# Kernel optimization log

Measured on AMD Instinct MI355X. Metric: run time of the kernel, lower is better.

## Reference

```python
import jax, jax.numpy as jnp
import numpy as np
from jax import lax

DN = ('NCHW', 'OIHW', 'NCHW')


def setup_inputs() -> dict:
    key = jax.random.key(0)
    k1, k2, k3, k4, k5, k6 = jax.random.split(key, 6)
    B, Ch, H, W = 16, 256, 32, 32   # two feature maps of 256 ch -> c = 512
    C = 2 * Ch
    return {
        'x1': jax.random.normal(k1, (B, Ch, H, W), dtype=jnp.float32),
        'x2': jax.random.normal(k2, (B, Ch, H, W), dtype=jnp.float32),
        'g_w': jax.random.normal(k3, (C, C, 3, 3), dtype=jnp.float32) * 0.02,
        'w_w': jax.random.normal(k4, (256, C, 1, 1), dtype=jnp.float32) * 0.05,
        'weight1': jax.random.normal(k5, (C, 16), dtype=jnp.float32) * 0.1,
        'weight2': jax.random.normal(k6, (C, 16), dtype=jnp.float32) * 0.1,
    }


def reference(x1, x2, g_w, w_w, weight1, weight2):
    x = jnp.concatenate([x1, x2], axis=1)            # [b, c, h, w]
    b, c, h, w = x.shape
    g_x = lax.conv_general_dilated(x, g_w, (1, 1), 'SAME', dimension_numbers=DN)
    value = g_x.reshape(b, c, h * w)                 # [b, c, n]
    q = x.reshape(b, c, h * w)                       # query == key source
    sim = jnp.einsum('bcn,bdn->bcd', q, q) * (float(c) ** -0.5)  # [b, c, c]
    random_map = weight1 @ weight2.T                 # [c, c]
    attn = jax.nn.softmax(sim + random_map[None], axis=-1)
    ctx = jnp.einsum('bcd,bdn->bcn', attn, value).reshape(b, c, h, w)
    out = lax.conv_general_dilated(ctx, w_w, (1, 1), 'VALID', dimension_numbers=DN)
    return out
```

## Files before the change

kernel.cpp:

```cpp
#include <hip/hip_runtime.h>
#include <math.h>

typedef float f32x4 __attribute__((ext_vector_type(4)));
typedef short s16x8 __attribute__((ext_vector_type(8)));
typedef unsigned int u32;
typedef unsigned short u16;
typedef u16 u16x4 __attribute__((ext_vector_type(4)));

static constexpr size_t OFF_XT    = 0;
static constexpr size_t OFF_XQ    = 4734976;
static constexpr size_t OFF_ATTNT = 4734976;
static constexpr size_t OFF_WATTN = 6832128;
static constexpr size_t OFF_P0    = 8929280;
static constexpr size_t OFF_P1    = 11026432;
static constexpr size_t OFF_VT    = 8929280;
static constexpr size_t OFF_WA    = 13123584;
static constexpr size_t OFF_RM    = 14303232;
static constexpr size_t OFF_WWB   = 14565376;

__device__ __forceinline__ u16 f2bf(float f) {
    u32 u = __float_as_uint(f);
    u32 r = (u + 0x7FFFu + ((u >> 16) & 1u)) >> 16;
    return (u16)r;
}
__device__ __forceinline__ float bf2f(u16 v) {
    return __uint_as_float(((u32)v) << 16);
}

__device__ __forceinline__ void gload_lds16(const void* g, void* l) {
    __builtin_amdgcn_global_load_lds(
        (const u32 __attribute__((address_space(1)))*)(uintptr_t)g,
        (u32 __attribute__((address_space(3)))*)(uintptr_t)l, 16, 0, 0);
}

__global__ __launch_bounds__(256) void prep_kernel(const float* __restrict__ x1,
                                                   const float* __restrict__ x2,
                                                   const float* __restrict__ gw,
                                                   const float* __restrict__ ww,
                                                   const float* __restrict__ w1,
                                                   const float* __restrict__ w2,
                                                   float* __restrict__ rm,
                                                   u16* __restrict__ wA,
                                                   u16* __restrict__ wwb,
                                                   u16* __restrict__ xT,
                                                   u16* __restrict__ xq) {
    __shared__ __attribute__((aligned(16))) u32 shm[4608];
    const int t = threadIdx.x;
    const int bid = blockIdx.x;

    if (bid < 512) {
        const int co = bid;
        const float* g = gw + (size_t)co * 4608;
        float* lf = (float*)shm;
#pragma unroll
        for (int i = 0; i < 18; ++i) lf[t + i * 256] = g[t + i * 256];
        __syncthreads();
        u16* dst = wA + (size_t)co * 4608;
#pragma unroll
        for (int i = 0; i < 18; ++i) {
            int k = t + i * 256;
            int r = k >> 9, ci = k & 511;
            dst[k] = f2bf(lf[ci * 9 + r]);
        }
    } else if (bid < 2560) {
        int xid = bid - 512;
        int nt = xid & 15;
        int cit = (xid >> 4) & 7;
        int b = xid >> 7;
        int n0 = nt * 64, ci0 = cit * 64;
        const float* src = (ci0 < 256) ? (x1 + ((size_t)(b * 256 + ci0)) * 1024)
                                       : (x2 + ((size_t)(b * 256 + ci0 - 256)) * 1024);
        u16* xqb = xq + ((size_t)(b * 512 + ci0)) * 1024;
        u16* lt = (u16*)shm;
#pragma unroll
        for (int p4 = 0; p4 < 4; ++p4) {
            int ch = (t >> 4) + p4 * 16;
            int px = (t & 15) * 4;
            float4 v = *(const float4*)&src[(size_t)ch * 1024 + n0 + px];
            u16x4 pk = {f2bf(v.x), f2bf(v.y), f2bf(v.z), f2bf(v.w)};
            *(u16x4*)&xqb[(size_t)ch * 1024 + n0 + px] = pk;
            lt[(px + 0) * 65 + ch] = pk[0];
            lt[(px + 1) * 65 + ch] = pk[1];
            lt[(px + 2) * 65 + ch] = pk[2];
            lt[(px + 3) * 65 + ch] = pk[3];
        }
        __syncthreads();
        {
            int px_l = t >> 2, c16 = (t & 3) * 16;
            int n = n0 + px_l;
            int y = n >> 5, x = n & 31;
            int p = (y + 1) * 34 + (x + 1);
            u16* dst = xT + ((size_t)b * 1156 + p) * 512 + ci0 + c16;
            *(s16x8*)&dst[0] = *(const s16x8*)&lt[px_l * 65 + c16];
            *(s16x8*)&dst[8] = *(const s16x8*)&lt[px_l * 65 + c16 + 8];
        }
    } else if (bid < 2576) {
        int b = bid - 2560;
        u16* base = xT + (size_t)b * 1156 * 512;
        s16x8 z = {0, 0, 0, 0, 0, 0, 0, 0};
        for (int idx = t; idx < 132 * 64; idx += 256) {
            int row = idx >> 6, seg = idx & 63;
            int p;
            if (row < 34) p = row;
            else if (row < 68) p = 1122 + (row - 34);
            else if (row < 100) p = (row - 67) * 34;
            else p = (row - 99) * 34 + 33;
            *(s16x8*)&base[(size_t)p * 512 + seg * 8] = z;
        }
    } else if (bid < 3600) {
        int idx = (bid - 2576) * 256 + t;
        int c = idx >> 9, d = idx & 511;
        float s = 0.f;
#pragma unroll
        for (int k = 0; k < 16; ++k) s = fmaf(w1[c * 16 + k], w2[d * 16 + k], s);
        rm[idx] = s;
    } else {
        int idx = (bid - 3600) * 256 + t;
        float4 v = ((const float4*)ww)[idx];
        u16x4 pk = {f2bf(v.x), f2bf(v.y), f2bf(v.z), f2bf(v.w)};
        *(u16x4*)&wwb[(size_t)idx * 4] = pk;
    }
}

__global__ __launch_bounds__(256) void sim_part(const u16* __restrict__ xq,
                                                u16* __restrict__ simP) {
    __shared__ __attribute__((aligned(16))) u16 smem[128 * 128];
    u16* As = smem;
    u16* Bs = smem + 128 * 64;
    const int b = blockIdx.z, m0 = blockIdx.y * 128;
    const int n0 = (blockIdx.x & 3) * 128, khalf = blockIdx.x >> 2;
    const int t = threadIdx.x, w = t >> 6, l = t & 63;
    const u16* xb = xq + (size_t)b * 512 * 1024 + khalf * 512;

    const u16 *agp[4], *bgp[4];
    u16 *ald[4], *bld[4];
#pragma unroll
    for (int i = 0; i < 4; ++i) {
        int rr = w * 8 + i * 32 + (l >> 3);
        int gi = (l & 7) ^ (rr & 7);
        agp[i] = xb + (size_t)(m0 + rr) * 1024 + gi * 8;
        bgp[i] = xb + (size_t)(n0 + rr) * 1024 + gi * 8;
        ald[i] = &As[(w * 8 + i * 32) * 64];
        bld[i] = &Bs[(w * 8 + i * 32) * 64];
    }

    f32x4 acc[4][4] = {};
    const int wm = (w >> 1) * 64, wn = (w & 1) * 64;

    for (int kt = 0; kt < 8; ++kt) {
        int ko = kt << 6;
        if (kt) __syncthreads();
#pragma unroll
        for (int i = 0; i < 4; ++i) gload_lds16(agp[i] + ko, ald[i]);
#pragma unroll
        for (int i = 0; i < 4; ++i) gload_lds16(bgp[i] + ko, bld[i]);
        __syncthreads();
#pragma unroll
        for (int kk = 0; kk < 2; ++kk) {
            int gbase = kk * 4 + (l >> 4);
            s16x8 af[4], bf[4];
#pragma unroll
            for (int i = 0; i < 4; ++i) {
                int row = wm + i * 16 + (l & 15);
                af[i] = *(const s16x8*)&As[row * 64 + ((gbase ^ (row & 7)) << 3)];
            }
#pragma unroll
            for (int j = 0; j < 4; ++j) {
                int row = wn + j * 16 + (l & 15);
                bf[j] = *(const s16x8*)&Bs[row * 64 + ((gbase ^ (row & 7)) << 3)];
            }
#pragma unroll
            for (int i = 0; i < 4; ++i)
#pragma unroll
                for (int j = 0; j < 4; ++j)
                    acc[i][j] = __builtin_amdgcn_mfma_f32_16x16x32_bf16(af[i], bf[j], acc[i][j], 0, 0, 0);
        }
    }

    __syncthreads();
    const int col = l & 15, r4 = (l >> 4) * 4;
#pragma unroll
    for (int i = 0; i < 4; ++i)
#pragma unroll
        for (int j = 0; j < 4; ++j) {
            int n_l = wn + j * 16 + col;
            int m_b = wm + i * 16 + r4;
            u16x4 pk = {f2bf(acc[i][j][0]), f2bf(acc[i][j][1]),
                        f2bf(acc[i][j][2]), f2bf(acc[i][j][3])};
            *(u16x4*)&smem[n_l * 128 + (m_b ^ ((n_l & 15) << 3))] = pk;
        }
    __syncthreads();
    u16* sTb = simP + (size_t)khalf * 4194304 + (size_t)b * 512 * 512;
    {
        int n_l = t >> 1;
#pragma unroll
        for (int rep = 0; rep < 8; ++rep) {
            int c0 = (((t & 1) + rep * 2) << 3);
            s16x8 v = *(const s16x8*)&smem[n_l * 128 + (c0 ^ ((n_l & 15) << 3))];
            *(s16x8*)&sTb[(size_t)(n0 + n_l) * 512 + m0 + c0] = v;
        }
    }
}

__global__ __launch_bounds__(256) void finish_kernel(const u16* __restrict__ p0,
                                                     const u16* __restrict__ p1,
                                                     const float* __restrict__ rm,
                                                     u16* __restrict__ attnT) {
    __shared__ float rml[32 * 513];
    __shared__ float scr[256];
    const int t = threadIdx.x;
    const int b = blockIdx.x >> 4, c0 = (blockIdx.x & 15) * 32;
    const int cl = t & 31, g = t >> 5;
    const float scale = 0.04419417382415922f;

    for (int idx = t; idx < 32 * 512; idx += 256) {
        int c_l = idx >> 9, d = idx & 511;
        rml[c_l * 513 + d] = rm[(size_t)(c0 + c_l) * 512 + d];
    }
    __syncthreads();

    const u16* q0 = p0 + (size_t)b * 262144 + c0 + cl;
    const u16* q1 = p1 + (size_t)b * 262144 + c0 + cl;
    u16* ap = attnT + (size_t)b * 262144 + c0 + cl;
    const float* rp = &rml[cl * 513];

    float e[64];
    float s = 0.f;
#pragma unroll
    for (int dd = 0; dd < 64; ++dd) {
        int d = g * 64 + dd;
        float v = (bf2f(q0[(size_t)d * 512]) + bf2f(q1[(size_t)d * 512])) * scale + rp[d];
        e[dd] = __expf(v);
        s += e[dd];
    }
    scr[t] = s;
    __syncthreads();
    float tot = 0.f;
#pragma unroll
    for (int k = 0; k < 8; ++k) tot += scr[k * 32 + cl];
    float inv = 1.f / tot;
#pragma unroll
    for (int dd = 0; dd < 64; ++dd) {
        int d = g * 64 + dd;
        ap[(size_t)d * 512] = f2bf(e[dd] * inv);
    }
}

__global__ __launch_bounds__(256) void conv_gemm(const u16* __restrict__ wA,
                                                 const u16* __restrict__ xT,
                                                 u16* __restrict__ vT) {
    __shared__ __attribute__((aligned(16))) u16 smem[128 * 128];
    u16* As = smem;
    u16* Bs = smem + 128 * 64;
    const int b = blockIdx.z, m0 = blockIdx.y * 128, n0 = blockIdx.x * 128;
    const int t = threadIdx.x, w = t >> 6, l = t & 63;
    const u16* xTb = xT + (size_t)b * 1156 * 512;

    int gi[4], pb[4];
    const u16* agp[4];
    u16 *ald[4], *bld[4];
#pragma unroll
    for (int i = 0; i < 4; ++i) {
        int rr = w * 8 + i * 32 + (l >> 3);
        gi[i] = (l & 7) ^ (rr & 7);
        agp[i] = wA + (size_t)(m0 + rr) * 4608 + gi[i] * 8;
        int n = n0 + rr;
        pb[i] = (n >> 5) * 34 + (n & 31);
        ald[i] = &As[(w * 8 + i * 32) * 64];
        bld[i] = &Bs[(w * 8 + i * 32) * 64];
    }

    f32x4 acc[4][4] = {};
    const int wm = (w >> 1) * 64, wn = (w & 1) * 64;

    for (int kt = 0; kt < 72; ++kt) {
        int r = kt >> 3, ci0k = (kt & 7) << 6;
        int rdiv3 = (r * 11) >> 5;
        int poff = rdiv3 * 34 + (r - rdiv3 * 3);
        int aofs = r * 512 + ci0k;
        if (kt) __syncthreads();
#pragma unroll
        for (int i = 0; i < 4; ++i) gload_lds16(agp[i] + aofs, ald[i]);
#pragma unroll
        for (int i = 0; i < 4; ++i)
            gload_lds16(xTb + (size_t)(pb[i] + poff) * 512 + ci0k + gi[i] * 8, bld[i]);
        __syncthreads();

#pragma unroll
        for (int kk = 0; kk < 2; ++kk) {
            int gbase = kk * 4 + (l >> 4);
            s16x8 af[4], bf[4];
#pragma unroll
            for (int i = 0; i < 4; ++i) {
                int row = wm + i * 16 + (l & 15);
                af[i] = *(const s16x8*)&As[row * 64 + ((gbase ^ (row & 7)) << 3)];
            }
#pragma unroll
            for (int j = 0; j < 4; ++j) {
                int row = wn + j * 16 + (l & 15);
                bf[j] = *(const s16x8*)&Bs[row * 64 + ((gbase ^ (row & 7)) << 3)];
            }
#pragma unroll
            for (int i = 0; i < 4; ++i)
#pragma unroll
                for (int j = 0; j < 4; ++j)
                    acc[i][j] = __builtin_amdgcn_mfma_f32_16x16x32_bf16(af[i], bf[j], acc[i][j], 0, 0, 0);
        }
    }

    __syncthreads();
    const int col = l & 15, r4 = (l >> 4) * 4;
#pragma unroll
    for (int i = 0; i < 4; ++i)
#pragma unroll
        for (int j = 0; j < 4; ++j) {
            int n_l = wn + j * 16 + col;
            int co_b = wm + i * 16 + r4;
            u16x4 pk = {f2bf(acc[i][j][0]), f2bf(acc[i][j][1]),
                        f2bf(acc[i][j][2]), f2bf(acc[i][j][3])};
            *(u16x4*)&smem[n_l * 128 + (co_b ^ ((n_l & 15) << 3))] = pk;
        }
    __syncthreads();
    u16* vTb = vT + (size_t)b * 1024 * 512;
    {
        int n_l = t >> 1;
#pragma unroll
        for (int rep = 0; rep < 8; ++rep) {
            int c0 = (((t & 1) + rep * 2) << 3);
            s16x8 v = *(const s16x8*)&smem[n_l * 128 + (c0 ^ ((n_l & 15) << 3))];
            *(s16x8*)&vTb[(size_t)(n0 + n_l) * 512 + m0 + c0] = v;
        }
    }
}

template <int MODE>
__global__ __launch_bounds__(256) void gemm_nt(const u16* __restrict__ A, size_t sA,
                                               const u16* __restrict__ B, size_t sB,
                                               void* __restrict__ Cv, size_t sC,
                                               int K, int ldc) {
    __shared__ __attribute__((aligned(16))) u16 As[128 * 64];
    __shared__ __attribute__((aligned(16))) u16 Bs[128 * 64];
    const int b = blockIdx.z, m0 = blockIdx.y * 128, n0 = blockIdx.x * 128;
    const int t = threadIdx.x, w = t >> 6, l = t & 63;
    const u16* Ab = A + (size_t)b * sA;
    const u16* Bb = B + (size_t)b * sB;

    const u16 *agp[4], *bgp[4];
    u16 *ald[4], *bld[4];
#pragma unroll
    for (int i = 0; i < 4; ++i) {
        int rr = w * 8 + i * 32 + (l >> 3);
        int gi = (l & 7) ^ (rr & 7);
        agp[i] = Ab + (size_t)(m0 + rr) * K + gi * 8;
        bgp[i] = Bb + (size_t)(n0 + rr) * K + gi * 8;
        ald[i] = &As[(w * 8 + i * 32) * 64];
        bld[i] = &Bs[(w * 8 + i * 32) * 64];
    }

    f32x4 acc[4][4] = {};
    const int wm = (w >> 1) * 64, wn = (w & 1) * 64;
    const int nkt = K >> 6;
    for (int kt = 0; kt < nkt; ++kt) {
        int ko = kt << 6;
        if (kt) __syncthreads();
#pragma unroll
        for (int i = 0; i < 4; ++i) gload_lds16(agp[i] + ko, ald[i]);
#pragma unroll
        for (int i = 0; i < 4; ++i) gload_lds16(bgp[i] + ko, bld[i]);
        __syncthreads();
#pragma unroll
        for (int kk = 0; kk < 2; ++kk) {
            int gbase = kk * 4 + (l >> 4);
            s16x8 af[4], bf[4];
#pragma unroll
            for (int i = 0; i < 4; ++i) {
                int row = wm + i * 16 + (l & 15);
                af[i] = *(const s16x8*)&As[row * 64 + ((gbase ^ (row & 7)) << 3)];
            }
#pragma unroll
            for (int j = 0; j < 4; ++j) {
                int row = wn + j * 16 + (l & 15);
                bf[j] = *(const s16x8*)&Bs[row * 64 + ((gbase ^ (row & 7)) << 3)];
            }
#pragma unroll
            for (int i = 0; i < 4; ++i)
#pragma unroll
                for (int j = 0; j < 4; ++j)
                    acc[i][j] = __builtin_amdgcn_mfma_f32_16x16x32_bf16(af[i], bf[j], acc[i][j], 0, 0, 0);
        }
    }

    const int col = l & 15, r4 = (l >> 4) * 4;
#pragma unroll
    for (int i = 0; i < 4; ++i)
#pragma unroll
        for (int j = 0; j < 4; ++j)
#pragma unroll
            for (int reg = 0; reg < 4; ++reg) {
                int m = m0 + wm + i * 16 + r4 + reg;
                int n = n0 + wn + j * 16 + col;
                if (MODE == 1) {
                    u16* C = (u16*)Cv + (size_t)b * sC;
                    C[(size_t)m * ldc + n] = f2bf(acc[i][j][reg]);
                } else {
                    float* C = (float*)Cv + (size_t)b * sC;
                    C[(size_t)m * ldc + n] = acc[i][j][reg];
                }
            }
}

extern "C" void kernel_launch(void* const* d_in, const int* in_sizes, int n_in,
                              void* d_out, int out_size, void* d_ws, size_t ws_size,
                              hipStream_t stream) {
    (void)in_sizes; (void)n_in; (void)out_size; (void)ws_size;
    const float* x1 = (const float*)d_in[0];
    const float* x2 = (const float*)d_in[1];
    const float* gw = (const float*)d_in[2];
    const float* ww = (const float*)d_in[3];
    const float* w1 = (const float*)d_in[4];
    const float* w2 = (const float*)d_in[5];
    float* out = (float*)d_out;
    float* ws = (float*)d_ws;

    u16* xT    = (u16*)(ws + OFF_XT);
    u16* xq    = (u16*)(ws + OFF_XQ);
    u16* attnT = (u16*)(ws + OFF_ATTNT);
    u16* wattn = (u16*)(ws + OFF_WATTN);
    u16* simP  = (u16*)(ws + OFF_P0);
    u16* p0    = (u16*)(ws + OFF_P0);
    u16* p1    = (u16*)(ws + OFF_P1);
    u16* vT    = (u16*)(ws + OFF_VT);
    u16* wA    = (u16*)(ws + OFF_WA);
    float* rm  = ws + OFF_RM;
    u16* wwb   = (u16*)(ws + OFF_WWB);

    prep_kernel<<<3728, 256, 0, stream>>>(x1, x2, gw, ww, w1, w2, rm, wA, wwb, xT, xq);
    sim_part<<<dim3(8, 4, 16), 256, 0, stream>>>(xq, simP);
    finish_kernel<<<256, 256, 0, stream>>>(p0, p1, rm, attnT);
    gemm_nt<1><<<dim3(4, 2, 16), 256, 0, stream>>>(
        wwb, 0, attnT, (size_t)512 * 512, wattn, (size_t)256 * 512, 512, 512);
    conv_gemm<<<dim3(8, 4, 16), 256, 0, stream>>>(wA, xT, vT);
    gemm_nt<2><<<dim3(8, 2, 16), 256, 0, stream>>>(
        wattn, (size_t)256 * 512, vT, (size_t)1024 * 512, out, (size_t)256 * 1024, 512, 1024);
}
```

Measured before the change: 222.3 us.

## Fuse sim and conv GEMMs into one concurrent launch with separate vT buffer

Merges the similarity partial GEMM and the 3x3 conv implicit GEMM into a single launch, splitting the grid by blockIdx.x so both sets of blocks run concurrently. vT moves to its own workspace region so it no longer aliases the sim partial buffers that finish_kernel reads. The aim is to fill the GPU better, overlap the two independent GEMMs and drop one launch. The fused path needs a larger workspace and falls back to the old sequence when the workspace is too small.

Result: slower. 275.2 us (+23.8%).

```diff
diff --git a/kernel.cpp b/kernel.cpp
--- a/kernel.cpp
+++ b/kernel.cpp
@@ -17,6 +17,7 @@
 static constexpr size_t OFF_WA    = 13123584;
 static constexpr size_t OFF_RM    = 14303232;
 static constexpr size_t OFF_WWB   = 14565376;
+static constexpr size_t OFF_VT2   = 14630912;
 
 __device__ __forceinline__ u16 f2bf(float f) {
     u32 u = __float_as_uint(f);
@@ -122,13 +123,14 @@
     }
 }
 
-__global__ __launch_bounds__(256) void sim_part(const u16* __restrict__ xq,
-                                                u16* __restrict__ simP) {
-    __shared__ __attribute__((aligned(16))) u16 smem[128 * 128];
+__device__ __forceinline__ void sim_body(u16* __restrict__ smem,
+                                         const u16* __restrict__ xq,
+                                         u16* __restrict__ simP,
+                                         int bx, int by, int bz) {
     u16* As = smem;
     u16* Bs = smem + 128 * 64;
-    const int b = blockIdx.z, m0 = blockIdx.y * 128;
-    const int n0 = (blockIdx.x & 3) * 128, khalf = blockIdx.x >> 2;
+    const int b = bz, m0 = by * 128;
+    const int n0 = (bx & 3) * 128, khalf = bx >> 2;
     const int t = threadIdx.x, w = t >> 6, l = t & 63;
     const u16* xb = xq + (size_t)b * 512 * 1024 + khalf * 512;
 
@@ -200,6 +202,118 @@
             *(s16x8*)&sTb[(size_t)(n0 + n_l) * 512 + m0 + c0] = v;
         }
     }
+}
+
+__device__ __forceinline__ void conv_body(u16* __restrict__ smem,
+                                          const u16* __restrict__ wA,
+                                          const u16* __restrict__ xT,
+                                          u16* __restrict__ vT,
+                                          int bx, int by, int bz) {
+    u16* As = smem;
+    u16* Bs = smem + 128 * 64;
+    const int b = bz, m0 = by * 128, n0 = bx * 128;
+    const int t = threadIdx.x, w = t >> 6, l = t & 63;
+    const u16* xTb = xT + (size_t)b * 1156 * 512;
+
+    int gi[4], pb[4];
+    const u16* agp[4];
+    u16 *ald[4], *bld[4];
+#pragma unroll
+    for (int i = 0; i < 4; ++i) {
+        int rr = w * 8 + i * 32 + (l >> 3);
+        gi[i] = (l & 7) ^ (rr & 7);
+        agp[i] = wA + (size_t)(m0 + rr) * 4608 + gi[i] * 8;
+        int n = n0 + rr;
+        pb[i] = (n >> 5) * 34 + (n & 31);
+        ald[i] = &As[(w * 8 + i * 32) * 64];
+        bld[i] = &Bs[(w * 8 + i * 32) * 64];
+    }
+
+    f32x4 acc[4][4] = {};
+    const int wm = (w >> 1) * 64, wn = (w & 1) * 64;
+
+    for (int kt = 0; kt < 72; ++kt) {
+        int r = kt >> 3, ci0k = (kt & 7) << 6;
+        int rdiv3 = (r * 11) >> 5;
+        int poff = rdiv3 * 34 + (r - rdiv3 * 3);
+        int aofs = r * 512 + ci0k;
+        if (kt) __syncthreads();
+#pragma unroll
+        for (int i = 0; i < 4; ++i) gload_lds16(agp[i] + aofs, ald[i]);
+#pragma unroll
+        for (int i = 0; i < 4; ++i)
+            gload_lds16(xTb + (size_t)(pb[i] + poff) * 512 + ci0k + gi[i] * 8, bld[i]);
+        __syncthreads();
+
+#pragma unroll
+        for (int kk = 0; kk < 2; ++kk) {
+            int gbase = kk * 4 + (l >> 4);
+            s16x8 af[4], bf[4];
+#pragma unroll
+            for (int i = 0; i < 4; ++i) {
+                int row = wm + i * 16 + (l & 15);
+                af[i] = *(const s16x8*)&As[row * 64 + ((gbase ^ (row & 7)) << 3)];
+            }
+#pragma unroll
+            for (int j = 0; j < 4; ++j) {
+                int row = wn + j * 16 + (l & 15);
+                bf[j] = *(const s16x8*)&Bs[row * 64 + ((gbase ^ (row & 7)) << 3)];
+            }
+#pragma unroll
+            for (int i = 0; i < 4; ++i)
+#pragma unroll
+                for (int j = 0; j < 4; ++j)
+                    acc[i][j] = __builtin_amdgcn_mfma_f32_16x16x32_bf16(af[i], bf[j], acc[i][j], 0, 0, 0);
+        }
+    }
+
+    __syncthreads();
+    const int col = l & 15, r4 = (l >> 4) * 4;
+#pragma unroll
+    for (int i = 0; i < 4; ++i)
+#pragma unroll
+        for (int j = 0; j < 4; ++j) {
+            int n_l = wn + j * 16 + col;
+            int co_b = wm + i * 16 + r4;
+            u16x4 pk = {f2bf(acc[i][j][0]), f2bf(acc[i][j][1]),
+                        f2bf(acc[i][j][2]), f2bf(acc[i][j][3])};
+            *(u16x4*)&smem[n_l * 128 + (co_b ^ ((n_l & 15) << 3))] = pk;
+        }
+    __syncthreads();
+    u16* vTb = vT + (size_t)b * 1024 * 512;
+    {
+        int n_l = t >> 1;
+#pragma unroll
+        for (int rep = 0; rep < 8; ++rep) {
+            int c0 = (((t & 1) + rep * 2) << 3);
+            s16x8 v = *(const s16x8*)&smem[n_l * 128 + (c0 ^ ((n_l & 15) << 3))];
+            *(s16x8*)&vTb[(size_t)(n0 + n_l) * 512 + m0 + c0] = v;
+        }
+    }
+}
+
+__global__ __launch_bounds__(256) void sim_part(const u16* __restrict__ xq,
+                                                u16* __restrict__ simP) {
+    __shared__ __attribute__((aligned(16))) u16 smem[128 * 128];
+    sim_body(smem, xq, simP, blockIdx.x, blockIdx.y, blockIdx.z);
+}
+__global__ __launch_bounds__(256) void conv_gemm(const u16* __restrict__ wA,
+                                                 const u16* __restrict__ xT,
+                                                 u16* __restrict__ vT) {
+    __shared__ __attribute__((aligned(16))) u16 smem[128 * 128];
+    conv_body(smem, wA, xT, vT, blockIdx.x, blockIdx.y, blockIdx.z);
+}
+
+__global__ __launch_bounds__(256) void sim_conv_fused(const u16* __restrict__ xq,
+                                                      u16* __restrict__ simP,
+                                                      const u16* __restrict__ wA,
+                                                      const u16* __restrict__ xT,
+                                                      u16* __restrict__ vT) {
+    __shared__ __attribute__((aligned(16))) u16 smem[128 * 128];
+    if (blockIdx.x < 8)
+        conv_body(smem, wA, xT, vT, blockIdx.x, blockIdx.y, blockIdx.z);
+    else
+        sim_body(smem, xq, simP, blockIdx.x - 8, blockIdx.y, blockIdx.z);
 }
 
 __global__ __launch_bounds__(256) void finish_kernel(const u16* __restrict__ p0,
@@ -243,93 +357,6 @@
     for (int dd = 0; dd < 64; ++dd) {
         int d = g * 64 + dd;
         ap[(size_t)d * 512] = f2bf(e[dd] * inv);
-    }
-}
-
-__global__ __launch_bounds__(256) void conv_gemm(const u16* __restrict__ wA,
-                                                 const u16* __restrict__ xT,
-                                                 u16* __restrict__ vT) {
-    __shared__ __attribute__((aligned(16))) u16 smem[128 * 128];
-    u16* As = smem;
-    u16* Bs = smem + 128 * 64;
-    const int b = blockIdx.z, m0 = blockIdx.y * 128, n0 = blockIdx.x * 128;
-    const int t = threadIdx.x, w = t >> 6, l = t & 63;
-    const u16* xTb = xT + (size_t)b * 1156 * 512;
-
-    int gi[4], pb[4];
-    const u16* agp[4];
-    u16 *ald[4], *bld[4];
-#pragma unroll
-    for (int i = 0; i < 4; ++i) {
-        int rr = w * 8 + i * 32 + (l >> 3);
-        gi[i] = (l & 7) ^ (rr & 7);
-        agp[i] = wA + (size_t)(m0 + rr) * 4608 + gi[i] * 8;
-        int n = n0 + rr;
-        pb[i] = (n >> 5) * 34 + (n & 31);
-        ald[i] = &As[(w * 8 + i * 32) * 64];
-        bld[i] = &Bs[(w * 8 + i * 32) * 64];
-    }
-
-    f32x4 acc[4][4] = {};
-    const int wm = (w >> 1) * 64, wn = (w & 1) * 64;
-
-    for (int kt = 0; kt < 72; ++kt) {
-        int r = kt >> 3, ci0k = (kt & 7) << 6;
-        int rdiv3 = (r * 11) >> 5;
-        int poff = rdiv3 * 34 + (r - rdiv3 * 3);
-        int aofs = r * 512 + ci0k;
-        if (kt) __syncthreads();
-#pragma unroll
-        for (int i = 0; i < 4; ++i) gload_lds16(agp[i] + aofs, ald[i]);
-#pragma unroll
-        for (int i = 0; i < 4; ++i)
-            gload_lds16(xTb + (size_t)(pb[i] + poff) * 512 + ci0k + gi[i] * 8, bld[i]);
-        __syncthreads();
-
-#pragma unroll
-        for (int kk = 0; kk < 2; ++kk) {
-            int gbase = kk * 4 + (l >> 4);
-            s16x8 af[4], bf[4];
-#pragma unroll
-            for (int i = 0; i < 4; ++i) {
-                int row = wm + i * 16 + (l & 15);
-                af[i] = *(const s16x8*)&As[row * 64 + ((gbase ^ (row & 7)) << 3)];
-            }
-#pragma unroll
-            for (int j = 0; j < 4; ++j) {
-                int row = wn + j * 16 + (l & 15);
-                bf[j] = *(const s16x8*)&Bs[row * 64 + ((gbase ^ (row & 7)) << 3)];
-            }
-#pragma unroll
-            for (int i = 0; i < 4; ++i)
-#pragma unroll
-                for (int j = 0; j < 4; ++j)
-                    acc[i][j] = __builtin_amdgcn_mfma_f32_16x16x32_bf16(af[i], bf[j], acc[i][j], 0, 0, 0);
-        }
-    }
-
-    __syncthreads();
-    const int col = l & 15, r4 = (l >> 4) * 4;
-#pragma unroll
-    for (int i = 0; i < 4; ++i)
-#pragma unroll
-        for (int j = 0; j < 4; ++j) {
-            int n_l = wn + j * 16 + col;
-            int co_b = wm + i * 16 + r4;
-            u16x4 pk = {f2bf(acc[i][j][0]), f2bf(acc[i][j][1]),
-                        f2bf(acc[i][j][2]), f2bf(acc[i][j][3])};
-            *(u16x4*)&smem[n_l * 128 + (co_b ^ ((n_l & 15) << 3))] = pk;
-        }
-    __syncthreads();
-    u16* vTb = vT + (size_t)b * 1024 * 512;
-    {
-        int n_l = t >> 1;
-#pragma unroll
-        for (int rep = 0; rep < 8; ++rep) {
-            int c0 = (((t & 1) + rep * 2) << 3);
-            s16x8 v = *(const s16x8*)&smem[n_l * 128 + (c0 ^ ((n_l & 15) << 3))];
-            *(s16x8*)&vTb[(size_t)(n0 + n_l) * 512 + m0 + c0] = v;
-        }
     }
 }
 
@@ -412,7 +439,7 @@
 extern "C" void kernel_launch(void* const* d_in, const int* in_sizes, int n_in,
                               void* d_out, int out_size, void* d_ws, size_t ws_size,
                               hipStream_t stream) {
-    (void)in_sizes; (void)n_in; (void)out_size; (void)ws_size;
+    (void)in_sizes; (void)n_in; (void)out_size;
     const float* x1 = (const float*)d_in[0];
     const float* x2 = (const float*)d_in[1];
     const float* gw = (const float*)d_in[2];
@@ -429,17 +456,28 @@
     u16* simP  = (u16*)(ws + OFF_P0);
     u16* p0    = (u16*)(ws + OFF_P0);
     u16* p1    = (u16*)(ws + OFF_P1);
-    u16* vT    = (u16*)(ws + OFF_VT);
     u16* wA    = (u16*)(ws + OFF_WA);
     float* rm  = ws + OFF_RM;
     u16* wwb   = (u16*)(ws + OFF_WWB);
 
+    const bool roomy = ws_size >= (size_t)75300864;
+    u16* vT = roomy ? (u16*)(ws + OFF_VT2) : (u16*)(ws + OFF_VT);
+
     prep_kernel<<<3728, 256, 0, stream>>>(x1, x2, gw, ww, w1, w2, rm, wA, wwb, xT, xq);
-    sim_part<<<dim3(8, 4, 16), 256, 0, stream>>>(xq, simP);
+
+    if (roomy) {
+        sim_conv_fused<<<dim3(16, 4, 16), 256, 0, stream>>>(xq, simP, wA, xT, vT);
+    } else {
+        sim_part<<<dim3(8, 4, 16), 256, 0, stream>>>(xq, simP);
+    }
+
     finish_kernel<<<256, 256, 0, stream>>>(p0, p1, rm, attnT);
     gemm_nt<1><<<dim3(4, 2, 16), 256, 0, stream>>>(
         wwb, 0, attnT, (size_t)512 * 512, wattn, (size_t)256 * 512, 512, 512);
-    conv_gemm<<<dim3(8, 4, 16), 256, 0, stream>>>(wA, xT, vT);
+
+    if (!roomy)
+        conv_gemm<<<dim3(8, 4, 16), 256, 0, stream>>>(wA, xT, vT);
+
     gemm_nt<2><<<dim3(8, 2, 16), 256, 0, stream>>>(
         wattn, (size_t)256 * 512, vT, (size_t)1024 * 512, out, (size_t)256 * 1024, 512, 1024);
 }
```

## Split conv GEMM K dimension in two and fold reduction into final GEMM

Applied to the files above, without the earlier changes.

The 3x3 conv GEMM (K=4608) is split into two halves computed by separate blocks, doubling the grid from 512 to 1024 blocks to improve CU occupancy. Each half writes a bf16 partial result to its own buffer, and the final attention-times-value GEMM consumes both partials by concatenating along K, so the sum happens for free via linearity. This costs an extra partial buffer write/read and extra bf16 rounding of partials, and only activates when the workspace is large enough.

Result: slower. 238.9 us (+7.5%).

```diff
diff --git a/kernel.cpp b/kernel.cpp
--- a/kernel.cpp
+++ b/kernel.cpp
@@ -17,6 +17,7 @@
 static constexpr size_t OFF_WA    = 13123584;
 static constexpr size_t OFF_RM    = 14303232;
 static constexpr size_t OFF_WWB   = 14565376;
+static constexpr size_t OFF_VT2   = 14630912;
 
 __device__ __forceinline__ u16 f2bf(float f) {
     u32 u = __float_as_uint(f);
@@ -246,6 +247,97 @@
     }
 }
 
+__global__ __launch_bounds__(256) void conv_split(const u16* __restrict__ wA,
+                                                  const u16* __restrict__ xT,
+                                                  u16* __restrict__ vT0,
+                                                  u16* __restrict__ vT1) {
+    __shared__ __attribute__((aligned(16))) u16 smem[128 * 128];
+    u16* As = smem;
+    u16* Bs = smem + 128 * 64;
+    const int b = blockIdx.z >> 1, kh = blockIdx.z & 1;
+    const int m0 = blockIdx.y * 128, n0 = blockIdx.x * 128;
+    const int t = threadIdx.x, w = t >> 6, l = t & 63;
+    const u16* xTb = xT + (size_t)b * 1156 * 512;
+    u16* vTd = (kh ? vT1 : vT0);
+
+    int gi[4], pb[4];
+    const u16* agp[4];
+    u16 *ald[4], *bld[4];
+#pragma unroll
+    for (int i = 0; i < 4; ++i) {
+        int rr = w * 8 + i * 32 + (l >> 3);
+        gi[i] = (l & 7) ^ (rr & 7);
+        agp[i] = wA + (size_t)(m0 + rr) * 4608 + gi[i] * 8;
+        int n = n0 + rr;
+        pb[i] = (n >> 5) * 34 + (n & 31);
+        ald[i] = &As[(w * 8 + i * 32) * 64];
+        bld[i] = &Bs[(w * 8 + i * 32) * 64];
+    }
+
+    f32x4 acc[4][4] = {};
+    const int wm = (w >> 1) * 64, wn = (w & 1) * 64;
+
+    for (int s = 0; s < 36; ++s) {
+        int kt = kh * 36 + s;
+        int r = kt >> 3, ci0k = (kt & 7) << 6;
+        int rdiv3 = (r * 11) >> 5;
+        int poff = rdiv3 * 34 + (r - rdiv3 * 3);
+        int aofs = r * 512 + ci0k;
+        if (s) __syncthreads();
+#pragma unroll
+        for (int i = 0; i < 4; ++i) gload_lds16(agp[i] + aofs, ald[i]);
+#pragma unroll
+        for (int i = 0; i < 4; ++i)
+            gload_lds16(xTb + (size_t)(pb[i] + poff) * 512 + ci0k + gi[i] * 8, bld[i]);
+        __syncthreads();
+
+#pragma unroll
+        for (int kk = 0; kk < 2; ++kk) {
+            int gbase = kk * 4 + (l >> 4);
+            s16x8 af[4], bf[4];
+#pragma unroll
+            for (int i = 0; i < 4; ++i) {
+                int row = wm + i * 16 + (l & 15);
+                af[i] = *(const s16x8*)&As[row * 64 + ((gbase ^ (row & 7)) << 3)];
+            }
+#pragma unroll
+            for (int j = 0; j < 4; ++j) {
+                int row = wn + j * 16 + (l & 15);
+                bf[j] = *(const s16x8*)&Bs[row * 64 + ((gbase ^ (row & 7)) << 3)];
+            }
+#pragma unroll
+            for (int i = 0; i < 4; ++i)
+#pragma unroll
+                for (int j = 0; j < 4; ++j)
+                    acc[i][j] = __builtin_amdgcn_mfma_f32_16x16x32_bf16(af[i], bf[j], acc[i][j], 0, 0, 0);
+        }
+    }
+
+    __syncthreads();
+    const int col = l & 15, r4 = (l >> 4) * 4;
+#pragma unroll
+    for (int i = 0; i < 4; ++i)
+#pragma unroll
+        for (int j = 0; j < 4; ++j) {
+            int n_l = wn + j * 16 + col;
+            int co_b = wm + i * 16 + r4;
+            u16x4 pk = {f2bf(acc[i][j][0]), f2bf(acc[i][j][1]),
+                        f2bf(acc[i][j][2]), f2bf(acc[i][j][3])};
+            *(u16x4*)&smem[n_l * 128 + (co_b ^ ((n_l & 15) << 3))] = pk;
+        }
+    __syncthreads();
+    u16* vTb = vTd + (size_t)b * 1024 * 512;
+    {
+        int n_l = t >> 1;
+#pragma unroll
+        for (int rep = 0; rep < 8; ++rep) {
+            int c0 = (((t & 1) + rep * 2) << 3);
+            s16x8 v = *(const s16x8*)&smem[n_l * 128 + (c0 ^ ((n_l & 15) << 3))];
+            *(s16x8*)&vTb[(size_t)(n0 + n_l) * 512 + m0 + c0] = v;
+        }
+    }
+}
+
 __global__ __launch_bounds__(256) void conv_gemm(const u16* __restrict__ wA,
                                                  const u16* __restrict__ xT,
                                                  u16* __restrict__ vT) {
@@ -409,10 +501,82 @@
             }
 }
 
+__global__ __launch_bounds__(256) void gemm_final2(const u16* __restrict__ A,
+                                                   const u16* __restrict__ B0,
+                                                   const u16* __restrict__ B1,
+                                                   float* __restrict__ C) {
+    __shared__ __attribute__((aligned(16))) u16 As[128 * 64];
+    __shared__ __attribute__((aligned(16))) u16 Bs[128 * 64];
+    const int b = blockIdx.z, m0 = blockIdx.y * 128, n0 = blockIdx.x * 128;
+    const int t = threadIdx.x, w = t >> 6, l = t & 63;
+    const u16* Ab = A + (size_t)b * 256 * 512;
+    const u16* B0b = B0 + (size_t)b * 1024 * 512;
+    const u16* B1b = B1 + (size_t)b * 1024 * 512;
+
+    const u16* agp[4];
+    size_t boff[4];
+    u16 *ald[4], *bld[4];
+#pragma unroll
+    for (int i = 0; i < 4; ++i) {
+        int rr = w * 8 + i * 32 + (l >> 3);
+        int gi = (l & 7) ^ (rr & 7);
+        agp[i] = Ab + (size_t)(m0 + rr) * 512 + gi * 8;
+        boff[i] = (size_t)(n0 + rr) * 512 + gi * 8;
+        ald[i] = &As[(w * 8 + i * 32) * 64];
+        bld[i] = &Bs[(w * 8 + i * 32) * 64];
+    }
+
+    f32x4 acc[4][4] = {};
+    const int wm = (w >> 1) * 64, wn = (w & 1) * 64;
+    for (int kt = 0; kt < 16; ++kt) {
+        int ko = (kt & 7) << 6;
+        const u16* Bb = (kt < 8) ? B0b : B1b;
+        if (kt) __syncthreads();
+#pragma unroll
+        for (int i = 0; i < 4; ++i) gload_lds16(agp[i] + ko, ald[i]);
+#pragma unroll
+        for (int i = 0; i < 4; ++i) gload_lds16(Bb + boff[i] + ko, bld[i]);
+        __syncthreads();
+#pragma unroll
+        for (int kk = 0; kk < 2; ++kk) {
+            int gbase = kk * 4 + (l >> 4);
+            s16x8 af[4], bf[4];
+#pragma unroll
+            for (int i = 0; i < 4; ++i) {
+                int row = wm + i * 16 + (l & 15);
+                af[i] = *(const s16x8*)&As[row * 64 + ((gbase ^ (row & 7)) << 3)];
+            }
+#pragma unroll
+            for (int j = 0; j < 4; ++j) {
+                int row = wn + j * 16 + (l & 15);
+                bf[j] = *(const s16x8*)&Bs[row * 64 + ((gbase ^ (row & 7)) << 3)];
+            }
+#pragma unroll
+            for (int i = 0; i < 4; ++i)
+#pragma unroll
+                for (int j = 0; j < 4; ++j)
+                    acc[i][j] = __builtin_amdgcn_mfma_f32_16x16x32_bf16(af[i], bf[j], acc[i][j], 0, 0, 0);
+        }
+    }
+
+    const int col = l & 15, r4 = (l >> 4) * 4;
+    float* Cb = C + (size_t)b * 256 * 1024;
+#pragma unroll
+    for (int i = 0; i < 4; ++i)
+#pragma unroll
+        for (int j = 0; j < 4; ++j)
+#pragma unroll
+            for (int reg = 0; reg < 4; ++reg) {
+                int m = m0 + wm + i * 16 + r4 + reg;
+                int n = n0 + wn + j * 16 + col;
+                Cb[(size_t)m * 1024 + n] = acc[i][j][reg];
+            }
+}
+
 extern "C" void kernel_launch(void* const* d_in, const int* in_sizes, int n_in,
                               void* d_out, int out_size, void* d_ws, size_t ws_size,
                               hipStream_t stream) {
-    (void)in_sizes; (void)n_in; (void)out_size; (void)ws_size;
+    (void)in_sizes; (void)n_in; (void)out_size;
     const float* x1 = (const float*)d_in[0];
     const float* x2 = (const float*)d_in[1];
     const float* gw = (const float*)d_in[2];
@@ -429,17 +593,26 @@
     u16* simP  = (u16*)(ws + OFF_P0);
     u16* p0    = (u16*)(ws + OFF_P0);
     u16* p1    = (u16*)(ws + OFF_P1);
-    u16* vT    = (u16*)(ws + OFF_VT);
+    u16* vT0   = (u16*)(ws + OFF_VT);
+    u16* vT1   = (u16*)(ws + OFF_VT2);
     u16* wA    = (u16*)(ws + OFF_WA);
     float* rm  = ws + OFF_RM;
     u16* wwb   = (u16*)(ws + OFF_WWB);
+
+    const bool splitk = ws_size >= (size_t)75300864;
 
     prep_kernel<<<3728, 256, 0, stream>>>(x1, x2, gw, ww, w1, w2, rm, wA, wwb, xT, xq);
     sim_part<<<dim3(8, 4, 16), 256, 0, stream>>>(xq, simP);
     finish_kernel<<<256, 256, 0, stream>>>(p0, p1, rm, attnT);
     gemm_nt<1><<<dim3(4, 2, 16), 256, 0, stream>>>(
         wwb, 0, attnT, (size_t)512 * 512, wattn, (size_t)256 * 512, 512, 512);
-    conv_gemm<<<dim3(8, 4, 16), 256, 0, stream>>>(wA, xT, vT);
-    gemm_nt<2><<<dim3(8, 2, 16), 256, 0, stream>>>(
-        wattn, (size_t)256 * 512, vT, (size_t)1024 * 512, out, (size_t)256 * 1024, 512, 1024);
-}
+
+    if (splitk) {
+        conv_split<<<dim3(8, 4, 32), 256, 0, stream>>>(wA, xT, vT0, vT1);
+        gemm_final2<<<dim3(8, 2, 16), 256, 0, stream>>>(wattn, vT0, vT1, out);
+    } else {
+        conv_gemm<<<dim3(8, 4, 16), 256, 0, stream>>>(wA, xT, vT0);
+        gemm_nt<2><<<dim3(8, 2, 16), 256, 0, stream>>>(
+            wattn, (size_t)256 * 512, vT0, (size_t)1024 * 512, out, (size_t)256 * 1024, 512, 1024);
+    }
+}
```

## Rewrite conv GEMM as triple-buffered 256x128 tile with phased loads

Applied to the files above, without the earlier changes.

Replaces the 3x3 conv implicit GEMM kernel with a 512-thread version using a 256x128 output tile. A three-stage LDS ring holds the A and B tiles. Each tile's global-to-LDS loads are split across two phases and interleaved with the MFMA blocks, with manual vmcnt waits and raw barriers. MFMA sections run at raised wave priority. The aim is to hide global memory latency behind compute and improve operand reuse, at the cost of a large LDS footprint (one block per CU) and a halved grid of 256 blocks.

New measurement: 227.3 us. +2.3%, slower.

```diff
diff --git a/kernel.cpp b/kernel.cpp
--- a/kernel.cpp
+++ b/kernel.cpp
@@ -246,78 +246,140 @@
     }
 }
 
-__global__ __launch_bounds__(256) void conv_gemm(const u16* __restrict__ wA,
-                                                 const u16* __restrict__ xT,
-                                                 u16* __restrict__ vT) {
-    __shared__ __attribute__((aligned(16))) u16 smem[128 * 128];
-    u16* As = smem;
-    u16* Bs = smem + 128 * 64;
-    const int b = blockIdx.z, m0 = blockIdx.y * 128, n0 = blockIdx.x * 128;
+__global__ __launch_bounds__(512) void conv_8ph(const u16* __restrict__ wA,
+                                                const u16* __restrict__ xT,
+                                                u16* __restrict__ vT) {
+    __shared__ __attribute__((aligned(16))) u16 smem[73728];
+    const int b = blockIdx.z, m0 = blockIdx.y * 128, n0 = blockIdx.x * 256;
     const int t = threadIdx.x, w = t >> 6, l = t & 63;
     const u16* xTb = xT + (size_t)b * 1156 * 512;
 
-    int gi[4], pb[4];
-    const u16* agp[4];
-    u16 *ald[4], *bld[4];
+    const u16* agp[2];
+    int pbb[4], giB[4];
+#pragma unroll
+    for (int i = 0; i < 2; ++i) {
+        int rr = i * 64 + w * 8 + (l >> 3);
+        int gi = (l & 7) ^ (rr & 7);
+        agp[i] = wA + (size_t)(m0 + rr) * 4608 + gi * 8;
+    }
 #pragma unroll
     for (int i = 0; i < 4; ++i) {
-        int rr = w * 8 + i * 32 + (l >> 3);
-        gi[i] = (l & 7) ^ (rr & 7);
-        agp[i] = wA + (size_t)(m0 + rr) * 4608 + gi[i] * 8;
+        int rr = i * 64 + w * 8 + (l >> 3);
         int n = n0 + rr;
-        pb[i] = (n >> 5) * 34 + (n & 31);
-        ald[i] = &As[(w * 8 + i * 32) * 64];
-        bld[i] = &Bs[(w * 8 + i * 32) * 64];
-    }
+        pbb[i] = (n >> 5) * 34 + (n & 31);
+        giB[i] = (l & 7) ^ (rr & 7);
+    }
+
+    auto stage_tile = [&](int kt, u16* dA, u16* dB) {
+        int r = kt >> 3, ci0 = (kt & 7) << 6;
+        int rd3 = (r * 11) >> 5;
+        int poff = rd3 * 34 + (r - rd3 * 3);
+        int aofs = r * 512 + ci0;
+        gload_lds16(agp[0] + aofs, dA + (w * 8) * 64);
+        gload_lds16(agp[1] + aofs, dA + (64 + w * 8) * 64);
+        gload_lds16(xTb + (size_t)(pbb[0] + poff) * 512 + ci0 + giB[0] * 8, dB + (w * 8) * 64);
+        gload_lds16(xTb + (size_t)(pbb[1] + poff) * 512 + ci0 + giB[1] * 8, dB + (64 + w * 8) * 64);
+        gload_lds16(xTb + (size_t)(pbb[2] + poff) * 512 + ci0 + giB[2] * 8, dB + (128 + w * 8) * 64);
+        gload_lds16(xTb + (size_t)(pbb[3] + poff) * 512 + ci0 + giB[3] * 8, dB + (192 + w * 8) * 64);
+    };
+
+    stage_tile(0, smem, smem + 8192);
+    stage_tile(1, smem + 24576, smem + 24576 + 8192);
 
     f32x4 acc[4][4] = {};
-    const int wm = (w >> 1) * 64, wn = (w & 1) * 64;
-
-    for (int kt = 0; kt < 72; ++kt) {
-        int r = kt >> 3, ci0k = (kt & 7) << 6;
-        int rdiv3 = (r * 11) >> 5;
-        int poff = rdiv3 * 34 + (r - rdiv3 * 3);
-        int aofs = r * 512 + ci0k;
-        if (kt) __syncthreads();
-#pragma unroll
-        for (int i = 0; i < 4; ++i) gload_lds16(agp[i] + aofs, ald[i]);
-#pragma unroll
-        for (int i = 0; i < 4; ++i)
-            gload_lds16(xTb + (size_t)(pb[i] + poff) * 512 + ci0k + gi[i] * 8, bld[i]);
-        __syncthreads();
-
-#pragma unroll
-        for (int kk = 0; kk < 2; ++kk) {
-            int gbase = kk * 4 + (l >> 4);
-            s16x8 af[4], bf[4];
-#pragma unroll
-            for (int i = 0; i < 4; ++i) {
-                int row = wm + i * 16 + (l & 15);
-                af[i] = *(const s16x8*)&As[row * 64 + ((gbase ^ (row & 7)) << 3)];
-            }
-#pragma unroll
-            for (int j = 0; j < 4; ++j) {
-                int row = wn + j * 16 + (l & 15);
-                bf[j] = *(const s16x8*)&Bs[row * 64 + ((gbase ^ (row & 7)) << 3)];
-            }
-#pragma unroll
-            for (int i = 0; i < 4; ++i)
-#pragma unroll
-                for (int j = 0; j < 4; ++j)
-                    acc[i][j] = __builtin_amdgcn_mfma_f32_16x16x32_bf16(af[i], bf[j], acc[i][j], 0, 0, 0);
-        }
+    const int wmo = (w >> 2) * 64, wno = (w & 3) * 64;
+    const int lr = l & 15, gb0 = l >> 4;
+
+    int cur = 0;
+    for (int j = 0; j < 72; ++j) {
+        int stg = cur + 2; if (stg >= 3) stg -= 3;
+        u16* cA = smem + cur * 24576;
+        u16* cB = cA + 8192;
+        u16* sA = smem + stg * 24576;
+        u16* sB = sA + 8192;
+        const bool dost = (j + 2) < 72;
+        int r2 = 0, ci02 = 0, poff2 = 0, aofs2 = 0;
+        if (dost) {
+            int kt2 = j + 2;
+            r2 = kt2 >> 3; ci02 = (kt2 & 7) << 6;
+            int rd3 = (r2 * 11) >> 5;
+            poff2 = rd3 * 34 + (r2 - rd3 * 3);
+            aofs2 = r2 * 512 + ci02;
+        }
+
+        if (j < 71) asm volatile("s_waitcnt vmcnt(6)" ::: "memory");
+        else        asm volatile("s_waitcnt vmcnt(0)" ::: "memory");
+        __builtin_amdgcn_s_barrier();
+
+        s16x8 af[4][2], bf[4][2];
+#pragma unroll
+        for (int mi = 0; mi < 4; ++mi) {
+            int row = wmo + mi * 16 + lr;
+#pragma unroll
+            for (int ks = 0; ks < 2; ++ks)
+                af[mi][ks] = *(const s16x8*)&cA[row * 64 + (((ks * 4 + gb0) ^ (row & 7)) << 3)];
+        }
+#pragma unroll
+        for (int q = 0; q < 2; ++q) {
+            int row = wno + q * 16 + lr;
+#pragma unroll
+            for (int ks = 0; ks < 2; ++ks)
+                bf[q][ks] = *(const s16x8*)&cB[row * 64 + (((ks * 4 + gb0) ^ (row & 7)) << 3)];
+        }
+        if (dost) {
+            gload_lds16(agp[0] + aofs2, sA + (w * 8) * 64);
+            gload_lds16(agp[1] + aofs2, sA + (64 + w * 8) * 64);
+            gload_lds16(xTb + (size_t)(pbb[0] + poff2) * 512 + ci02 + giB[0] * 8, sB + (w * 8) * 64);
+        }
+        __builtin_amdgcn_s_barrier();
+        __builtin_amdgcn_s_setprio(1);
+#pragma unroll
+        for (int ks = 0; ks < 2; ++ks)
+#pragma unroll
+            for (int q = 0; q < 2; ++q)
+#pragma unroll
+                for (int mi = 0; mi < 4; ++mi)
+                    acc[mi][q] = __builtin_amdgcn_mfma_f32_16x16x32_bf16(af[mi][ks], bf[q][ks], acc[mi][q], 0, 0, 0);
+        __builtin_amdgcn_s_setprio(0);
+        __builtin_amdgcn_s_barrier();
+
+#pragma unroll
+        for (int q = 2; q < 4; ++q) {
+            int row = wno + q * 16 + lr;
+#pragma unroll
+            for (int ks = 0; ks < 2; ++ks)
+                bf[q][ks] = *(const s16x8*)&cB[row * 64 + (((ks * 4 + gb0) ^ (row & 7)) << 3)];
+        }
+        if (dost) {
+            gload_lds16(xTb + (size_t)(pbb[1] + poff2) * 512 + ci02 + giB[1] * 8, sB + (64 + w * 8) * 64);
+            gload_lds16(xTb + (size_t)(pbb[2] + poff2) * 512 + ci02 + giB[2] * 8, sB + (128 + w * 8) * 64);
+            gload_lds16(xTb + (size_t)(pbb[3] + poff2) * 512 + ci02 + giB[3] * 8, sB + (192 + w * 8) * 64);
+        }
+        __builtin_amdgcn_s_barrier();
+        __builtin_amdgcn_s_setprio(1);
+#pragma unroll
+        for (int ks = 0; ks < 2; ++ks)
+#pragma unroll
+            for (int q = 2; q < 4; ++q)
+#pragma unroll
+                for (int mi = 0; mi < 4; ++mi)
+                    acc[mi][q] = __builtin_amdgcn_mfma_f32_16x16x32_bf16(af[mi][ks], bf[q][ks], acc[mi][q], 0, 0, 0);
+        __builtin_amdgcn_s_setprio(0);
+        __builtin_amdgcn_s_barrier();
+
+        cur += 1; if (cur >= 3) cur -= 3;
     }
 
     __syncthreads();
     const int col = l & 15, r4 = (l >> 4) * 4;
 #pragma unroll
-    for (int i = 0; i < 4; ++i)
-#pragma unroll
-        for (int j = 0; j < 4; ++j) {
-            int n_l = wn + j * 16 + col;
-            int co_b = wm + i * 16 + r4;
-            u16x4 pk = {f2bf(acc[i][j][0]), f2bf(acc[i][j][1]),
-                        f2bf(acc[i][j][2]), f2bf(acc[i][j][3])};
+    for (int mi = 0; mi < 4; ++mi)
+#pragma unroll
+        for (int nj = 0; nj < 4; ++nj) {
+            int n_l = wno + nj * 16 + col;
+            int co_b = wmo + mi * 16 + r4;
+            u16x4 pk = {f2bf(acc[mi][nj][0]), f2bf(acc[mi][nj][1]),
+                        f2bf(acc[mi][nj][2]), f2bf(acc[mi][nj][3])};
             *(u16x4*)&smem[n_l * 128 + (co_b ^ ((n_l & 15) << 3))] = pk;
         }
     __syncthreads();
@@ -439,7 +501,7 @@
     finish_kernel<<<256, 256, 0, stream>>>(p0, p1, rm, attnT);
     gemm_nt<1><<<dim3(4, 2, 16), 256, 0, stream>>>(
         wwb, 0, attnT, (size_t)512 * 512, wattn, (size_t)256 * 512, 512, 512);
-    conv_gemm<<<dim3(8, 4, 16), 256, 0, stream>>>(wA, xT, vT);
+    conv_8ph<<<dim3(4, 4, 16), 512, 0, stream>>>(wA, xT, vT);
     gemm_nt<2><<<dim3(8, 2, 16), 256, 0, stream>>>(
         wattn, (size_t)256 * 512, vT, (size_t)1024 * 512, out, (size_t)256 * 1024, 512, 1024);
 }
```
